# Optimization experiments

Measured on AMD Instinct MI355X. Metric: run time of the kernel, lower is better.

## Reference

```python
import jax, jax.numpy as jnp
import numpy as np

M, N = 24, 12
H1 = (M + N) * 10 * 8        # 2880
HID = (M * M + N * N) * 10   # 7200
H2 = M * N * 4               # 1152
DOUT = M * N                 # 288
EPS = 1e-12


def setup_inputs() -> dict:
    key = jax.random.key(0)
    ks = jax.random.split(key, 16)
    s = 0.02  # weight scale
    return {
        "yt": jax.random.normal(ks[0], (N,), jnp.float32),
        "F": jax.random.normal(ks[1], (M, M), jnp.float32) * 0.1,
        "Hm": jax.random.normal(ks[2], (N, M), jnp.float32) * 0.1,
        "m1x_posterior": jax.random.normal(ks[3], (M, 1), jnp.float32),
        "m1x_prior_old": jax.random.normal(ks[4], (M, 1), jnp.float32),
        "hn": jax.random.normal(ks[5], (HID,), jnp.float32),
        "W1": jax.random.normal(ks[6], (H1, M + N), jnp.float32) * s,
        "b1": jax.random.normal(ks[7], (H1,), jnp.float32) * s,
        "Wih": jax.random.normal(ks[8], (3 * HID, H1), jnp.float32) * s,
        "Whh": jax.random.normal(ks[9], (3 * HID, HID), jnp.float32) * s,
        "bih": jax.random.normal(ks[10], (3 * HID,), jnp.float32) * s,
        "bhh": jax.random.normal(ks[11], (3 * HID,), jnp.float32) * s,
        "W2": jax.random.normal(ks[12], (H2, HID), jnp.float32) * s,
        "b2": jax.random.normal(ks[13], (H2,), jnp.float32) * s,
        "W3": jax.random.normal(ks[14], (DOUT, H2), jnp.float32) * s,
        "b3": jax.random.normal(ks[15], (DOUT,), jnp.float32) * s,
    }


def _l2_normalize(x):
    # torch F.normalize(p=2, dim=0, eps=1e-12)
    return x / jnp.maximum(jnp.linalg.norm(x), EPS)


def _gru_cell(x, h, Wih, Whh, bih, bhh):
    gi = Wih @ x + bih            # [3*HID]
    gh = Whh @ h + bhh            # [3*HID]
    gi_r, gi_z, gi_n = jnp.split(gi, 3)
    gh_r, gh_z, gh_n = jnp.split(gh, 3)
    r = jax.nn.sigmoid(gi_r + gh_r)
    z = jax.nn.sigmoid(gi_z + gh_z)
    n = jnp.tanh(gi_n + r * gh_n)
    return (1.0 - z) * n + z * h


def reference(yt, F, Hm, m1x_posterior, m1x_prior_old, hn,
              W1, b1, Wih, Whh, bih, bhh, W2, b2, W3, b3):
    # step_prior
    m1x_prior = F @ m1x_posterior        # [M,1]
    m1y = Hm @ m1x_prior                 # [N,1]
    # step_KGain_est
    dm1x = _l2_normalize((m1x_posterior - m1x_prior_old)[:, 0])  # [M]
    dm1y = _l2_normalize(yt - m1y[:, 0])                         # [N]
    kg_in = jnp.concatenate([dm1y, dm1x])                        # [M+N]
    l1 = jax.nn.relu(W1 @ kg_in + b1)                            # [H1]
    h_new = _gru_cell(l1, hn, Wih, Whh, bih, bhh)                # [HID]
    l2 = jax.nn.relu(W2 @ h_new + b2)                            # [H2]
    kg = (W3 @ l2 + b3).reshape(M, N)                            # Kalman gain
    # KNet_step update
    dy = yt[:, None] - m1y                                       # [N,1]
    m1x_post_new = m1x_prior + kg @ dy                           # [M,1]
    return m1x_post_new[:, 0]
```

## Files before the change

### kernel.cpp

```cpp
#include <hip/hip_runtime.h>
#include <math.h>

#define M_DIM 24
#define N_DIM 12
#define H1    2880
#define HID   7200
#define H2    1152
#define DOUT  288
#define KGIN  (M_DIM + N_DIM)

#define WS_PRIOR 0
#define WS_DY    96
#define WS_L1    128
#define WS_HNEW  3072
#define WS_L2    10304
#define WS_GI    11520
#define WS_GH    33152

typedef float floatx4 __attribute__((ext_vector_type(4)));

__device__ __forceinline__ float wave_sum(float v) {
    #pragma unroll
    for (int o = 32; o; o >>= 1) v += __shfl_xor(v, o);
    return v;
}

__device__ __forceinline__ floatx4 ntload(const float4* p) {
    return __builtin_nontemporal_load((const floatx4*)p);
}

__global__ __launch_bounds__(256) void k_l1h(
        const float* __restrict__ yt, const float* __restrict__ F,
        const float* __restrict__ Hm, const float* __restrict__ post,
        const float* __restrict__ prior_old,
        const float* __restrict__ W1, const float* __restrict__ b1,
        float* __restrict__ ws) {
    __shared__ float s_prior[M_DIM];
    __shared__ float s_m1y[N_DIM];
    __shared__ float s_x[KGIN];
    __shared__ float s_dy[N_DIM];
    int t = threadIdx.x, lane = t & 63, w = t >> 6;

    if (t < M_DIM) {
        float acc = 0.f;
        #pragma unroll
        for (int j = 0; j < M_DIM; ++j) acc += F[t * M_DIM + j] * post[j];
        s_prior[t] = acc;
    }
    __syncthreads();
    if (t < N_DIM) {
        float acc = 0.f;
        #pragma unroll
        for (int j = 0; j < M_DIM; ++j) acc += Hm[t * M_DIM + j] * s_prior[j];
        s_m1y[t] = acc;
    }
    __syncthreads();
    if (w == 0) {
        float vx = 0.f;
        if (lane < M_DIM) vx = post[lane] - prior_old[lane];
        float nx = fmaxf(sqrtf(wave_sum(vx * vx)), 1e-12f);
        float vy = 0.f;
        if (lane < N_DIM) vy = yt[lane] - s_m1y[lane];
        float ny = fmaxf(sqrtf(wave_sum(vy * vy)), 1e-12f);
        if (lane < N_DIM) { s_x[lane] = vy / ny; s_dy[lane] = vy; }
        if (lane < M_DIM) s_x[N_DIM + lane] = vx / nx;
    }
    __syncthreads();

    if (blockIdx.x == 0) {
        if (t < M_DIM) ws[WS_PRIOR + t] = s_prior[t];
        if (t < N_DIM) ws[WS_DY + t] = s_dy[t];
    }

    int i = blockIdx.x * 4 + w;
    float acc = (lane < KGIN) ? W1[(size_t)i * KGIN + lane] * s_x[lane] : 0.f;
    acc = wave_sum(acc);
    if (lane == 0) ws[WS_L1 + i] = fmaxf(acc + b1[i], 0.f);
}

__global__ __launch_bounds__(256, 8) void k_gates(
        const float* __restrict__ Wih, const float* __restrict__ Whh,
        const float* __restrict__ bih, const float* __restrict__ bhh,
        const float* __restrict__ hn, float* __restrict__ ws) {
    int t = threadIdx.x, lane = t & 63, w = t >> 6;
    int b = blockIdx.x;
    int g = b >> 3, r = b & 7;
    if ((g & 1) == 0) {
        int i = ((g >> 1) * 8 + r) * 4 + w;
        const float4* xh = (const float4*)hn;
        const float4* ur = (const float4*)(Whh + (size_t)i * HID);
        const float4* uz = (const float4*)(Whh + (size_t)(i + HID) * HID);
        const float4* un = (const float4*)(Whh + (size_t)(i + 2 * HID) * HID);
        float hr = 0.f, hz = 0.f, hh = 0.f;
        #pragma unroll 2
        for (int kk = 0; kk < 28; ++kk) {
            int k = kk * 64 + lane;
            float4 x = xh[k];
            floatx4 a = ntload(ur + k), bb = ntload(uz + k), c = ntload(un + k);
            hr += a.x * x.x + a.y * x.y + a.z * x.z + a.w * x.w;
            hz += bb.x * x.x + bb.y * x.y + bb.z * x.z + bb.w * x.w;
            hh += c.x * x.x + c.y * x.y + c.z * x.z + c.w * x.w;
        }
        if (lane < 8) {
            int k = 28 * 64 + lane;
            float4 x = xh[k];
            floatx4 a = ntload(ur + k), bb = ntload(uz + k), c = ntload(un + k);
            hr += a.x * x.x + a.y * x.y + a.z * x.z + a.w * x.w;
            hz += bb.x * x.x + bb.y * x.y + bb.z * x.z + bb.w * x.w;
            hh += c.x * x.x + c.y * x.y + c.z * x.z + c.w * x.w;
        }
        hr = wave_sum(hr); hz = wave_sum(hz); hh = wave_sum(hh);
        if (lane == 0) {
            ws[WS_GH + i]           = hr + bhh[i];
            ws[WS_GH + HID + i]     = hz + bhh[i + HID];
            ws[WS_GH + 2 * HID + i] = hh + bhh[i + 2 * HID];
        }
    } else {
        int i = ((g >> 1) * 8 + r) * 4 + w;
        const float4* x1 = (const float4*)(ws + WS_L1);
        const float4* wr = (const float4*)(Wih + (size_t)i * H1);
        const float4* wz = (const float4*)(Wih + (size_t)(i + HID) * H1);
        const float4* wn = (const float4*)(Wih + (size_t)(i + 2 * HID) * H1);
        float ar = 0.f, az = 0.f, an = 0.f;
        #pragma unroll 2
        for (int kk = 0; kk < 11; ++kk) {
            int k = kk * 64 + lane;
            float4 x = x1[k];
            floatx4 a = ntload(wr + k), bb = ntload(wz + k), c = ntload(wn + k);
            ar += a.x * x.x + a.y * x.y + a.z * x.z + a.w * x.w;
            az += bb.x * x.x + bb.y * x.y + bb.z * x.z + bb.w * x.w;
            an += c.x * x.x + c.y * x.y + c.z * x.z + c.w * x.w;
        }
        if (lane < 16) {
            int k = 11 * 64 + lane;
            float4 x = x1[k];
            floatx4 a = ntload(wr + k), bb = ntload(wz + k), c = ntload(wn + k);
            ar += a.x * x.x + a.y * x.y + a.z * x.z + a.w * x.w;
            az += bb.x * x.x + bb.y * x.y + bb.z * x.z + bb.w * x.w;
            an += c.x * x.x + c.y * x.y + c.z * x.z + c.w * x.w;
        }
        ar = wave_sum(ar); az = wave_sum(az); an = wave_sum(an);
        if (lane == 0) {
            ws[WS_GI + i]           = ar + bih[i];
            ws[WS_GI + HID + i]     = az + bih[i + HID];
            ws[WS_GI + 2 * HID + i] = an + bih[i + 2 * HID];
        }
    }
}

__global__ __launch_bounds__(256) void k_comb(const float* __restrict__ hn,
                                              float* __restrict__ ws) {
    int i = blockIdx.x * 256 + threadIdx.x;
    if (i < HID) {
        float gr = ws[WS_GI + i] + ws[WS_GH + i];
        float gz = ws[WS_GI + HID + i] + ws[WS_GH + HID + i];
        float r = 1.f / (1.f + expf(-gr));
        float z = 1.f / (1.f + expf(-gz));
        float n = tanhf(ws[WS_GI + 2 * HID + i] + r * ws[WS_GH + 2 * HID + i]);
        ws[WS_HNEW + i] = (1.f - z) * n + z * hn[i];
    }
}

__global__ __launch_bounds__(256, 8) void k_l2(
        const float* __restrict__ W2, const float* __restrict__ b2,
        float* __restrict__ ws) {
    __shared__ float s_p[4];
    int t = threadIdx.x, lane = t & 63, w = t >> 6;
    int i = blockIdx.x;
    const float4* x4 = (const float4*)(ws + WS_HNEW);
    const float4* wr = (const float4*)(W2 + (size_t)i * HID);
    float acc = 0.f;
    #pragma unroll 2
    for (int kk = 0; kk < 7; ++kk) {
        int k = kk * 256 + t;
        float4 x = x4[k];
        floatx4 a = ntload(wr + k);
        acc += a.x * x.x + a.y * x.y + a.z * x.z + a.w * x.w;
    }
    if (t < 8) {
        int k = 7 * 256 + t;
        float4 x = x4[k];
        floatx4 a = ntload(wr + k);
        acc += a.x * x.x + a.y * x.y + a.z * x.z + a.w * x.w;
    }
    acc = wave_sum(acc);
    if (lane == 0) s_p[w] = acc;
    __syncthreads();
    if (t == 0)
        ws[WS_L2 + i] = fmaxf(s_p[0] + s_p[1] + s_p[2] + s_p[3] + b2[i], 0.f);
}

__global__ __launch_bounds__(768) void k_kg_out(
        const float* __restrict__ W3, const float* __restrict__ b3,
        const float* __restrict__ ws, float* __restrict__ out) {
    __shared__ float s_kg[N_DIM];
    int m = blockIdx.x;
    int t = threadIdx.x, lane = t & 63, w = t >> 6;
    int row = m * N_DIM + w;
    const float4* wr = (const float4*)(W3 + (size_t)row * H2);
    const float4* x4 = (const float4*)(ws + WS_L2);
    float acc = 0.f;
    #pragma unroll
    for (int kk = 0; kk < 4; ++kk) {
        int k = kk * 64 + lane;
        float4 x = x4[k];
        floatx4 a = ntload(wr + k);
        acc += a.x * x.x + a.y * x.y + a.z * x.z + a.w * x.w;
    }
    if (lane < 32) {
        int k = 4 * 64 + lane;
        float4 x = x4[k];
        floatx4 a = ntload(wr + k);
        acc += a.x * x.x + a.y * x.y + a.z * x.z + a.w * x.w;
    }
    acc = wave_sum(acc);
    if (lane == 0) s_kg[w] = acc + b3[row];
    __syncthreads();
    if (t == 0) {
        float a = ws[WS_PRIOR + m];
        #pragma unroll
        for (int n = 0; n < N_DIM; ++n) a += s_kg[n] * ws[WS_DY + n];
        out[m] = a;
    }
}

extern "C" void kernel_launch(void* const* d_in, const int* in_sizes, int n_in,
                              void* d_out, int out_size, void* d_ws, size_t ws_size,
                              hipStream_t stream) {
    const float* yt        = (const float*)d_in[0];
    const float* F         = (const float*)d_in[1];
    const float* Hm        = (const float*)d_in[2];
    const float* post      = (const float*)d_in[3];
    const float* prior_old = (const float*)d_in[4];
    const float* hn        = (const float*)d_in[5];
    const float* W1        = (const float*)d_in[6];
    const float* b1        = (const float*)d_in[7];
    const float* Wih       = (const float*)d_in[8];
    const float* Whh       = (const float*)d_in[9];
    const float* bih       = (const float*)d_in[10];
    const float* bhh       = (const float*)d_in[11];
    const float* W2        = (const float*)d_in[12];
    const float* b2        = (const float*)d_in[13];
    const float* W3        = (const float*)d_in[14];
    const float* b3        = (const float*)d_in[15];
    float* out = (float*)d_out;
    float* ws  = (float*)d_ws;

    k_l1h   <<<H1 / 4, 256, 0, stream>>>(yt, F, Hm, post, prior_old, W1, b1, ws);
    k_gates <<<2 * (HID / 4), 256, 0, stream>>>(Wih, Whh, bih, bhh, hn, ws);
    k_comb  <<<(HID + 255) / 256, 256, 0, stream>>>(hn, ws);
    k_l2    <<<H2, 256, 0, stream>>>(W2, b2, ws);
    k_kg_out<<<M_DIM, 768, 0, stream>>>(W3, b3, ws, out);
}
```

Baseline: 169.5 us.

## Split Whh GEMV across two K-halves to balance gate blocks; use cached loads

The recurrent-weight GEMV blocks in the gate kernel are split into two halves along the hidden dimension. Each half writes its own partial sums, and the combine kernel adds them, so the Whh blocks carry about the same load as the Wih blocks and the grid grows from 3600 to 5400 blocks. This targets the tail imbalance where long Whh rows dominated the kernel. Separately, the W2 and W3 loads switch from nontemporal to normal loads. In exchange the change adds extra workspace traffic for the partial sums and an extra read in the combine step.

```diff
diff --git a/kernel.cpp b/kernel.cpp
--- a/kernel.cpp
+++ b/kernel.cpp
@@ -16,6 +16,7 @@
 #define WS_L2    10304
 #define WS_GI    11520
 #define WS_GH    33152
+#define WS_GH2   54752
 
 typedef float floatx4 __attribute__((ext_vector_type(4)));
 
@@ -85,15 +86,20 @@
     int t = threadIdx.x, lane = t & 63, w = t >> 6;
     int b = blockIdx.x;
     int g = b >> 3, r = b & 7;
-    if ((g & 1) == 0) {
-        int i = ((g >> 1) * 8 + r) * 4 + w;
-        const float4* xh = (const float4*)hn;
-        const float4* ur = (const float4*)(Whh + (size_t)i * HID);
-        const float4* uz = (const float4*)(Whh + (size_t)(i + HID) * HID);
-        const float4* un = (const float4*)(Whh + (size_t)(i + 2 * HID) * HID);
+    int gm = g % 3;
+    if (gm < 2) {
+        int hb = ((g / 3) * 2 + gm) * 8 + r;
+        int half = (hb >= 1800) ? 1 : 0;
+        int Q = hb - half * 1800;
+        int i = Q * 4 + w;
+        int base = half * 900;
+        const float4* xh = (const float4*)hn + base;
+        const float4* ur = (const float4*)(Whh + (size_t)i * HID) + base;
+        const float4* uz = (const float4*)(Whh + (size_t)(i + HID) * HID) + base;
+        const float4* un = (const float4*)(Whh + (size_t)(i + 2 * HID) * HID) + base;
         float hr = 0.f, hz = 0.f, hh = 0.f;
         #pragma unroll 2
-        for (int kk = 0; kk < 28; ++kk) {
+        for (int kk = 0; kk < 14; ++kk) {
             int k = kk * 64 + lane;
             float4 x = xh[k];
             floatx4 a = ntload(ur + k), bb = ntload(uz + k), c = ntload(un + k);
@@ -101,8 +107,8 @@
             hz += bb.x * x.x + bb.y * x.y + bb.z * x.z + bb.w * x.w;
             hh += c.x * x.x + c.y * x.y + c.z * x.z + c.w * x.w;
         }
-        if (lane < 8) {
-            int k = 28 * 64 + lane;
+        if (lane < 4) {
+            int k = 14 * 64 + lane;
             float4 x = xh[k];
             floatx4 a = ntload(ur + k), bb = ntload(uz + k), c = ntload(un + k);
             hr += a.x * x.x + a.y * x.y + a.z * x.z + a.w * x.w;
@@ -111,12 +117,18 @@
         }
         hr = wave_sum(hr); hz = wave_sum(hz); hh = wave_sum(hh);
         if (lane == 0) {
-            ws[WS_GH + i]           = hr + bhh[i];
-            ws[WS_GH + HID + i]     = hz + bhh[i + HID];
-            ws[WS_GH + 2 * HID + i] = hh + bhh[i + 2 * HID];
+            if (half) {
+                ws[WS_GH2 + i]           = hr;
+                ws[WS_GH2 + HID + i]     = hz;
+                ws[WS_GH2 + 2 * HID + i] = hh;
+            } else {
+                ws[WS_GH + i]           = hr + bhh[i];
+                ws[WS_GH + HID + i]     = hz + bhh[i + HID];
+                ws[WS_GH + 2 * HID + i] = hh + bhh[i + 2 * HID];
+            }
         }
     } else {
-        int i = ((g >> 1) * 8 + r) * 4 + w;
+        int i = ((g / 3) * 8 + r) * 4 + w;
         const float4* x1 = (const float4*)(ws + WS_L1);
         const float4* wr = (const float4*)(Wih + (size_t)i * H1);
         const float4* wz = (const float4*)(Wih + (size_t)(i + HID) * H1);
@@ -152,11 +164,14 @@
                                               float* __restrict__ ws) {
     int i = blockIdx.x * 256 + threadIdx.x;
     if (i < HID) {
-        float gr = ws[WS_GI + i] + ws[WS_GH + i];
-        float gz = ws[WS_GI + HID + i] + ws[WS_GH + HID + i];
+        float ghr = ws[WS_GH + i]           + ws[WS_GH2 + i];
+        float ghz = ws[WS_GH + HID + i]     + ws[WS_GH2 + HID + i];
+        float ghn = ws[WS_GH + 2 * HID + i] + ws[WS_GH2 + 2 * HID + i];
+        float gr = ws[WS_GI + i] + ghr;
+        float gz = ws[WS_GI + HID + i] + ghz;
         float r = 1.f / (1.f + expf(-gr));
         float z = 1.f / (1.f + expf(-gz));
-        float n = tanhf(ws[WS_GI + 2 * HID + i] + r * ws[WS_GH + 2 * HID + i]);
+        float n = tanhf(ws[WS_GI + 2 * HID + i] + r * ghn);
         ws[WS_HNEW + i] = (1.f - z) * n + z * hn[i];
     }
 }
@@ -174,13 +189,13 @@
     for (int kk = 0; kk < 7; ++kk) {
         int k = kk * 256 + t;
         float4 x = x4[k];
-        floatx4 a = ntload(wr + k);
+        float4 a = wr[k];
         acc += a.x * x.x + a.y * x.y + a.z * x.z + a.w * x.w;
     }
     if (t < 8) {
         int k = 7 * 256 + t;
         float4 x = x4[k];
-        floatx4 a = ntload(wr + k);
+        float4 a = wr[k];
         acc += a.x * x.x + a.y * x.y + a.z * x.z + a.w * x.w;
     }
     acc = wave_sum(acc);
@@ -204,13 +219,13 @@
     for (int kk = 0; kk < 4; ++kk) {
         int k = kk * 64 + lane;
         float4 x = x4[k];
-        floatx4 a = ntload(wr + k);
+        float4 a = wr[k];
         acc += a.x * x.x + a.y * x.y + a.z * x.z + a.w * x.w;
     }
     if (lane < 32) {
         int k = 4 * 64 + lane;
         float4 x = x4[k];
-        floatx4 a = ntload(wr + k);
+        float4 a = wr[k];
         acc += a.x * x.x + a.y * x.y + a.z * x.z + a.w * x.w;
     }
     acc = wave_sum(acc);
@@ -247,7 +262,7 @@
     float* ws  = (float*)d_ws;
 
     k_l1h   <<<H1 / 4, 256, 0, stream>>>(yt, F, Hm, post, prior_old, W1, b1, ws);
-    k_gates <<<2 * (HID / 4), 256, 0, stream>>>(Wih, Whh, bih, bhh, hn, ws);
+    k_gates <<<5400, 256, 0, stream>>>(Wih, Whh, bih, bhh, hn, ws);
     k_comb  <<<(HID + 255) / 256, 256, 0, stream>>>(hn, ws);
     k_l2    <<<H2, 256, 0, stream>>>(W2, b2, ws);
     k_kg_out<<<M_DIM, 768, 0, stream>>>(W3, b3, ws, out);
```

Measured after the change: 157.2 us, median of 2. 7.3% less time.
